# Optimization experiments

Hardware: AMD Instinct MI355X
Metric: run time of the kernel (lower is better)

## Reference

```python
import jax, jax.numpy as jnp
import numpy as np

N_HEADS = 32
D_IN = 128 + 256 + 1024  # 1408
D_HID = 256
D_OUT = 3


def setup_inputs() -> dict:
    key = jax.random.key(0)
    k1, k2, k3, k4, k5 = jax.random.split(key, 5)
    B = 16384
    total_feat = jax.random.normal(k1, (B, D_IN), dtype=jnp.float32)
    # Stacked per-head parameters. Original zero-inits the second Linear;
    # we use small random values so the baseline exercises non-trivial math.
    s1 = 1.0 / np.sqrt(D_IN)
    s2 = 1.0 / np.sqrt(D_HID)
    W1 = jax.random.uniform(k2, (N_HEADS, D_IN, D_HID), jnp.float32, -s1, s1)
    b1 = jax.random.uniform(k3, (N_HEADS, D_HID), jnp.float32, -s1, s1)
    W2 = jax.random.uniform(k4, (N_HEADS, D_HID, D_OUT), jnp.float32, -s2, s2)
    b2 = jax.random.uniform(k5, (N_HEADS, D_OUT), jnp.float32, -s2, s2)
    return {"total_feat": total_feat, "W1": W1, "b1": b1, "W2": W2, "b2": b2}


def reference(total_feat, W1, b1, W2, b2):
    # 32 heads of Linear(1408->256) -> ReLU -> Linear(256->3), batched.
    h = jax.nn.relu(jnp.einsum('bf,hfo->bho', total_feat, W1) + b1)  # [B,32,256]
    out = jnp.einsum('bho,hop->bhp', h, W2) + b2                     # [B,32,3]
    B = total_feat.shape[0]
    # concat(dim=-1) over heads == reshape since each head emits 3 contiguous values
    return out.reshape(B, N_HEADS * D_OUT)                           # [B,96]
```

## Files before the change

### kernel.cpp

```cpp
#include <hip/hip_runtime.h>
#include <hip/hip_bf16.h>
#include <stdint.h>

#define D_IN    1408
#define D_HID   256
#define N_HEADS 32
#define BATCH   16384

#define BM 64
#define BN 256
#define BK 64
#define KTILES (D_IN / BK)

typedef unsigned short u16;
typedef short short8 __attribute__((ext_vector_type(8)));
typedef float f32x4 __attribute__((ext_vector_type(4)));

__device__ __forceinline__ u16 f2b(float f) {
  __hip_bfloat16 h = __float2bfloat16(f);
  return *(u16*)&h;
}

__device__ __forceinline__ void gload_lds16(const void* g, void* l) {
  __builtin_amdgcn_global_load_lds(
      (const __attribute__((address_space(1))) uint32_t*)((const uint32_t*)g),
      (__attribute__((address_space(3))) uint32_t*)((uint32_t*)l),
      16, 0, 0);
}

__global__ void convert_x(const float4* __restrict__ X, ushort4* __restrict__ Xb) {
  int i = blockIdx.x * blockDim.x + threadIdx.x;
  float4 v = X[i];
  ushort4 o;
  o.x = f2b(v.x); o.y = f2b(v.y); o.z = f2b(v.z); o.w = f2b(v.w);
  Xb[i] = o;
}

__global__ void transpose_w1(const float* __restrict__ W1, u16* __restrict__ W1T) {
  __shared__ u16 tile[64][65];
  const int h = blockIdx.z;
  const int f0 = blockIdx.x * 64;
  const int o0 = blockIdx.y * 64;
  const int tx = threadIdx.x;
  const int ty = threadIdx.y;
  const size_t ib = (size_t)h * D_IN * D_HID;
  #pragma unroll
  for (int i = ty; i < 64; i += 4)
    tile[i][tx] = f2b(W1[ib + (size_t)(f0 + i) * D_HID + o0 + tx]);
  __syncthreads();
  const size_t ob = (size_t)h * D_HID * D_IN;
  #pragma unroll
  for (int i = ty; i < 64; i += 4)
    W1T[ob + (size_t)(o0 + i) * D_IN + f0 + tx] = tile[tx][i];
}

__global__ __launch_bounds__(256, 4) void mano_gemm(
    const u16* __restrict__ X,
    const u16* __restrict__ W1T,
    const float* __restrict__ b1,
    const float* __restrict__ W2,
    const float* __restrict__ b2,
    float* __restrict__ out)
{
  __shared__ __align__(16) u16 As[BM * BK];
  __shared__ __align__(16) u16 Bs[BN * BK];

  const int tid  = threadIdx.x;
  const int lane = tid & 63;
  const int wid  = tid >> 6;
  const int quad = lane >> 4;
  const int l15  = lane & 15;

  const int id    = blockIdx.x;
  const int xcd   = id & 7;
  const int s     = id >> 3;
  const int head  = xcd * 4 + (s & 3);
  const int mtile = s >> 2;
  const int m0    = mtile * BM;

  const u16* Au = X + (size_t)m0 * D_IN;
  const u16* Bu = W1T + (size_t)head * D_HID * D_IN;

  int aoff[2];
  #pragma unroll
  for (int c = 0; c < 2; ++c) {
    int ci  = c * 256 + wid * 64 + lane;
    int row = ci >> 3;
    int k8  = (ci & 7) ^ (row & 7);
    aoff[c] = row * D_IN + k8 * 8;
  }
  int boff[8];
  #pragma unroll
  for (int c = 0; c < 8; ++c) {
    int ci  = c * 256 + wid * 64 + lane;
    int row = ci >> 3;
    int k8  = (ci & 7) ^ (row & 7);
    boff[c] = row * D_IN + k8 * 8;
  }

  f32x4 acc[4][4];
  #pragma unroll
  for (int i = 0; i < 4; ++i)
    #pragma unroll
    for (int j = 0; j < 4; ++j)
      acc[i][j] = f32x4{0.f, 0.f, 0.f, 0.f};

  int arow[4], brow[4];
  #pragma unroll
  for (int i = 0; i < 4; ++i) {
    arow[i] = i * 16 + l15;
    brow[i] = wid * 64 + i * 16 + l15;
  }

  for (int kt = 0; kt < KTILES; ++kt) {
    const int kb = kt * BK;
    __syncthreads();
    #pragma unroll
    for (int c = 0; c < 2; ++c)
      gload_lds16(Au + aoff[c] + kb, As + (c * 256 + wid * 64) * 8);
    #pragma unroll
    for (int c = 0; c < 8; ++c)
      gload_lds16(Bu + boff[c] + kb, Bs + (c * 256 + wid * 64) * 8);
    __builtin_amdgcn_s_waitcnt(0x0F70);
    __syncthreads();

    #pragma unroll
    for (int ks = 0; ks < 2; ++ks) {
      short8 af[4], bfr[4];
      #pragma unroll
      for (int i = 0; i < 4; ++i) {
        int k8a = (ks * 4 + quad) ^ (arow[i] & 7);
        af[i]  = *(const short8*)((const char*)As + arow[i] * 128 + k8a * 16);
        int k8b = (ks * 4 + quad) ^ (brow[i] & 7);
        bfr[i] = *(const short8*)((const char*)Bs + brow[i] * 128 + k8b * 16);
      }
      #pragma unroll
      for (int i = 0; i < 4; ++i)
        #pragma unroll
        for (int j = 0; j < 4; ++j)
          acc[i][j] = __builtin_amdgcn_mfma_f32_16x16x32_bf16(af[i], bfr[j], acc[i][j], 0, 0, 0);
    }
  }

  const float* b1h = b1 + head * D_HID;
  const float* W2h = W2 + (size_t)head * D_HID * 3;

  float b1v[4], w2v[4][3];
  #pragma unroll
  for (int j = 0; j < 4; ++j) {
    int n = brow[j];
    b1v[j] = b1h[n];
    #pragma unroll
    for (int p = 0; p < 3; ++p)
      w2v[j][p] = W2h[n * 3 + p];
  }

  __syncthreads();
  float* scr = (float*)As;

  #pragma unroll
  for (int i = 0; i < 4; ++i) {
    float ps[4][3];
    #pragma unroll
    for (int r = 0; r < 4; ++r)
      #pragma unroll
      for (int p = 0; p < 3; ++p) ps[r][p] = 0.f;

    #pragma unroll
    for (int j = 0; j < 4; ++j)
      #pragma unroll
      for (int r = 0; r < 4; ++r) {
        float h = acc[i][j][r] + b1v[j];
        h = h > 0.f ? h : 0.f;
        #pragma unroll
        for (int p = 0; p < 3; ++p)
          ps[r][p] = fmaf(h, w2v[j][p], ps[r][p]);
      }

    #pragma unroll
    for (int mask = 1; mask < 16; mask <<= 1)
      #pragma unroll
      for (int r = 0; r < 4; ++r)
        #pragma unroll
        for (int p = 0; p < 3; ++p)
          ps[r][p] += __shfl_xor(ps[r][p], mask, 64);

    if (l15 == 0) {
      int row = i * 16 + quad * 4;
      #pragma unroll
      for (int r = 0; r < 4; ++r)
        #pragma unroll
        for (int p = 0; p < 3; ++p)
          scr[wid * 192 + (row + r) * 3 + p] = ps[r][p];
    }
  }
  __syncthreads();

  if (tid < 192) {
    int rl = tid / 3, p = tid - rl * 3;
    float v = scr[rl * 3 + p] + scr[192 + rl * 3 + p]
            + scr[384 + rl * 3 + p] + scr[576 + rl * 3 + p]
            + b2[head * 3 + p];
    out[(size_t)(m0 + rl) * (N_HEADS * 3) + head * 3 + p] = v;
  }
}

extern "C" void kernel_launch(void* const* d_in, const int* in_sizes, int n_in,
                              void* d_out, int out_size, void* d_ws, size_t ws_size,
                              hipStream_t stream) {
  const float* X  = (const float*)d_in[0];
  const float* W1 = (const float*)d_in[1];
  const float* b1 = (const float*)d_in[2];
  const float* W2 = (const float*)d_in[3];
  const float* b2 = (const float*)d_in[4];

  u16* Xb  = (u16*)d_ws;
  u16* W1T = (u16*)((char*)d_ws + (size_t)BATCH * D_IN * 2);

  convert_x<<<(BATCH * D_IN / 4) / 256, 256, 0, stream>>>(
      (const float4*)X, (ushort4*)Xb);

  transpose_w1<<<dim3(D_IN / 64, D_HID / 64, N_HEADS), dim3(64, 4), 0, stream>>>(W1, W1T);

  mano_gemm<<<dim3(BATCH / BM * N_HEADS), 256, 0, stream>>>(
      Xb, W1T, b1, W2, b2, (float*)d_out);
}
```

Measured before the change: 604.8 us.

## Enlarge GEMM tile to 256x256 with double-buffered LDS and interleaved MFMA phases

The tile grows from 64x256 to 256x256, the block from 256 to 512 threads (8 waves in a 2x4 grid), and LDS becomes double-buffered so global-to-LDS loads for the next K tiles overlap MFMA work. Each K iteration is split into four phases that alternate fragment loads, staged async copies, barriers and setprio around MFMA batches. The aim is more reuse of each loaded A and B element per MFMA and hidden global load latency. In exchange it uses more registers and LDS (128 KB), lowers occupancy, launches fewer blocks, and relies on fragile hand-counted vmcnt waits.

```diff
diff --git a/kernel.cpp b/kernel.cpp
--- a/kernel.cpp
+++ b/kernel.cpp
@@ -7,7 +7,7 @@
 #define N_HEADS 32
 #define BATCH   16384
 
-#define BM 64
+#define BM 256
 #define BN 256
 #define BK 64
 #define KTILES (D_IN / BK)
@@ -54,7 +54,7 @@
     W1T[ob + (size_t)(o0 + i) * D_IN + f0 + tx] = tile[tx][i];
 }
 
-__global__ __launch_bounds__(256, 4) void mano_gemm(
+__global__ __launch_bounds__(512, 2) void mano_gemm(
     const u16* __restrict__ X,
     const u16* __restrict__ W1T,
     const float* __restrict__ b1,
@@ -62,14 +62,16 @@
     const float* __restrict__ b2,
     float* __restrict__ out)
 {
-  __shared__ __align__(16) u16 As[BM * BK];
-  __shared__ __align__(16) u16 Bs[BN * BK];
+  __shared__ __align__(16) u16 As[2][BM * BK];
+  __shared__ __align__(16) u16 Bs[2][BN * BK];
 
   const int tid  = threadIdx.x;
   const int lane = tid & 63;
   const int wid  = tid >> 6;
   const int quad = lane >> 4;
   const int l15  = lane & 15;
+  const int wm   = wid >> 2;
+  const int wn   = wid & 3;
 
   const int id    = blockIdx.x;
   const int xcd   = id & 7;
@@ -81,85 +83,163 @@
   const u16* Au = X + (size_t)m0 * D_IN;
   const u16* Bu = W1T + (size_t)head * D_HID * D_IN;
 
-  int aoff[2];
+  int off[2][2];
   #pragma unroll
   for (int c = 0; c < 2; ++c) {
-    int ci  = c * 256 + wid * 64 + lane;
-    int row = ci >> 3;
-    int k8  = (ci & 7) ^ (row & 7);
-    aoff[c] = row * D_IN + k8 * 8;
-  }
-  int boff[8];
-  #pragma unroll
-  for (int c = 0; c < 8; ++c) {
-    int ci  = c * 256 + wid * 64 + lane;
-    int row = ci >> 3;
-    int k8  = (ci & 7) ^ (row & 7);
-    boff[c] = row * D_IN + k8 * 8;
-  }
-
-  f32x4 acc[4][4];
-  #pragma unroll
-  for (int i = 0; i < 4; ++i)
+    int ci = c * 512 + tid;
+    int rl = ci >> 3;
+    int k8 = (ci & 7) ^ (rl & 7);
+    #pragma unroll
+    for (int h = 0; h < 2; ++h)
+      off[h][c] = (h * 128 + rl) * D_IN + k8 * 8;
+  }
+
+#define STAGE_A(bufi, h, kt) do {                                          \
+    _Pragma("unroll")                                                      \
+    for (int c = 0; c < 2; ++c)                                            \
+      gload_lds16(Au + off[h][c] + (kt) * BK,                              \
+                  &As[bufi][((h) * 1024 + c * 512 + wid * 64) * 8]);       \
+  } while (0)
+#define STAGE_B(bufi, h, kt) do {                                          \
+    _Pragma("unroll")                                                      \
+    for (int c = 0; c < 2; ++c)                                            \
+      gload_lds16(Bu + off[h][c] + (kt) * BK,                              \
+                  &Bs[bufi][((h) * 1024 + c * 512 + wid * 64) * 8]);       \
+  } while (0)
+
+  const int wm16l = wm * 16 + l15;
+  const int wn16l = wn * 16 + l15;
+  const int rx  = l15 & 7;
+  const int co0 = (quad ^ rx) * 16;
+  const int co1 = ((4 + quad) ^ rx) * 16;
+
+#define LDA_FRAG(mf, ks) \
+  (*(const short8*)(Ab + ((mf) * 32 + wm16l) * 128 + ((ks) ? co1 : co0)))
+#define LDB_FRAG(nf, ks) \
+  (*(const short8*)(Bb + (nf) * 8192 + wn16l * 128 + ((ks) ? co1 : co0)))
+
+  f32x4 acc[8][4];
+  #pragma unroll
+  for (int i = 0; i < 8; ++i)
     #pragma unroll
     for (int j = 0; j < 4; ++j)
       acc[i][j] = f32x4{0.f, 0.f, 0.f, 0.f};
 
-  int arow[4], brow[4];
-  #pragma unroll
-  for (int i = 0; i < 4; ++i) {
-    arow[i] = i * 16 + l15;
-    brow[i] = wid * 64 + i * 16 + l15;
-  }
-
-  for (int kt = 0; kt < KTILES; ++kt) {
-    const int kb = kt * BK;
-    __syncthreads();
-    #pragma unroll
-    for (int c = 0; c < 2; ++c)
-      gload_lds16(Au + aoff[c] + kb, As + (c * 256 + wid * 64) * 8);
-    #pragma unroll
-    for (int c = 0; c < 8; ++c)
-      gload_lds16(Bu + boff[c] + kb, Bs + (c * 256 + wid * 64) * 8);
-    __builtin_amdgcn_s_waitcnt(0x0F70);
-    __syncthreads();
-
-    #pragma unroll
-    for (int ks = 0; ks < 2; ++ks) {
-      short8 af[4], bfr[4];
-      #pragma unroll
-      for (int i = 0; i < 4; ++i) {
-        int k8a = (ks * 4 + quad) ^ (arow[i] & 7);
-        af[i]  = *(const short8*)((const char*)As + arow[i] * 128 + k8a * 16);
-        int k8b = (ks * 4 + quad) ^ (brow[i] & 7);
-        bfr[i] = *(const short8*)((const char*)Bs + brow[i] * 128 + k8b * 16);
-      }
-      #pragma unroll
-      for (int i = 0; i < 4; ++i)
-        #pragma unroll
-        for (int j = 0; j < 4; ++j)
-          acc[i][j] = __builtin_amdgcn_mfma_f32_16x16x32_bf16(af[i], bfr[j], acc[i][j], 0, 0, 0);
-    }
-  }
+  STAGE_A(0, 0, 0);
+  STAGE_B(0, 1, 0);
+  STAGE_A(0, 1, 0);
+  STAGE_B(0, 0, 0);
+  STAGE_A(1, 0, 1);
+  STAGE_B(1, 1, 1);
+  asm volatile("s_waitcnt vmcnt(4)" ::: "memory");
+  __builtin_amdgcn_s_barrier();
+
+  short8 a[4][2], b[4][2];
+
+  for (int t = 0; t < KTILES; ++t) {
+    const int buf = t & 1;
+    const char* Ab = (const char*)&As[buf][0];
+    const char* Bb = (const char*)&Bs[buf][0];
+
+    #pragma unroll
+    for (int mf = 0; mf < 4; ++mf) {
+      a[mf][0] = LDA_FRAG(mf, 0);
+      a[mf][1] = LDA_FRAG(mf, 1);
+    }
+    #pragma unroll
+    for (int nf = 0; nf < 2; ++nf) {
+      b[nf][0] = LDB_FRAG(nf, 0);
+      b[nf][1] = LDB_FRAG(nf, 1);
+    }
+    if (t + 1 < KTILES) STAGE_A(buf ^ 1, 1, t + 1);
+    __builtin_amdgcn_s_barrier();
+    __builtin_amdgcn_s_setprio(1);
+    #pragma unroll
+    for (int mf = 0; mf < 4; ++mf)
+      #pragma unroll
+      for (int nf = 0; nf < 2; ++nf) {
+        acc[mf][nf] = __builtin_amdgcn_mfma_f32_16x16x32_bf16(a[mf][0], b[nf][0], acc[mf][nf], 0, 0, 0);
+        acc[mf][nf] = __builtin_amdgcn_mfma_f32_16x16x32_bf16(a[mf][1], b[nf][1], acc[mf][nf], 0, 0, 0);
+      }
+    __builtin_amdgcn_s_setprio(0);
+    __builtin_amdgcn_s_barrier();
+
+    #pragma unroll
+    for (int nf = 2; nf < 4; ++nf) {
+      b[nf][0] = LDB_FRAG(nf, 0);
+      b[nf][1] = LDB_FRAG(nf, 1);
+    }
+    if (t + 1 < KTILES) STAGE_B(buf ^ 1, 0, t + 1);
+    __builtin_amdgcn_s_barrier();
+    __builtin_amdgcn_s_setprio(1);
+    #pragma unroll
+    for (int mf = 0; mf < 4; ++mf)
+      #pragma unroll
+      for (int nf = 2; nf < 4; ++nf) {
+        acc[mf][nf] = __builtin_amdgcn_mfma_f32_16x16x32_bf16(a[mf][0], b[nf][0], acc[mf][nf], 0, 0, 0);
+        acc[mf][nf] = __builtin_amdgcn_mfma_f32_16x16x32_bf16(a[mf][1], b[nf][1], acc[mf][nf], 0, 0, 0);
+      }
+    __builtin_amdgcn_s_setprio(0);
+    __builtin_amdgcn_s_barrier();
+
+    #pragma unroll
+    for (int i = 0; i < 4; ++i) {
+      a[i][0] = LDA_FRAG(4 + i, 0);
+      a[i][1] = LDA_FRAG(4 + i, 1);
+    }
+    if (t + 2 < KTILES) STAGE_A(buf, 0, t + 2);
+    __builtin_amdgcn_s_barrier();
+    __builtin_amdgcn_s_setprio(1);
+    #pragma unroll
+    for (int i = 0; i < 4; ++i)
+      #pragma unroll
+      for (int nf = 2; nf < 4; ++nf) {
+        acc[4 + i][nf] = __builtin_amdgcn_mfma_f32_16x16x32_bf16(a[i][0], b[nf][0], acc[4 + i][nf], 0, 0, 0);
+        acc[4 + i][nf] = __builtin_amdgcn_mfma_f32_16x16x32_bf16(a[i][1], b[nf][1], acc[4 + i][nf], 0, 0, 0);
+      }
+    __builtin_amdgcn_s_setprio(0);
+    __builtin_amdgcn_s_barrier();
+
+    if (t + 2 < KTILES) STAGE_B(buf, 1, t + 2);
+    __builtin_amdgcn_s_barrier();
+    __builtin_amdgcn_s_setprio(1);
+    #pragma unroll
+    for (int i = 0; i < 4; ++i)
+      #pragma unroll
+      for (int nf = 0; nf < 2; ++nf) {
+        acc[4 + i][nf] = __builtin_amdgcn_mfma_f32_16x16x32_bf16(a[i][0], b[nf][0], acc[4 + i][nf], 0, 0, 0);
+        acc[4 + i][nf] = __builtin_amdgcn_mfma_f32_16x16x32_bf16(a[i][1], b[nf][1], acc[4 + i][nf], 0, 0, 0);
+      }
+    __builtin_amdgcn_s_setprio(0);
+    if (t < KTILES - 2) {
+      asm volatile("s_waitcnt vmcnt(4)" ::: "memory");
+    } else {
+      asm volatile("s_waitcnt vmcnt(0)" ::: "memory");
+    }
+    __builtin_amdgcn_s_barrier();
+  }
+
+#undef STAGE_A
+#undef STAGE_B
+#undef LDA_FRAG
+#undef LDB_FRAG
 
   const float* b1h = b1 + head * D_HID;
   const float* W2h = W2 + (size_t)head * D_HID * 3;
 
   float b1v[4], w2v[4][3];
   #pragma unroll
-  for (int j = 0; j < 4; ++j) {
-    int n = brow[j];
-    b1v[j] = b1h[n];
-    #pragma unroll
-    for (int p = 0; p < 3; ++p)
-      w2v[j][p] = W2h[n * 3 + p];
-  }
-
-  __syncthreads();
-  float* scr = (float*)As;
-
-  #pragma unroll
-  for (int i = 0; i < 4; ++i) {
+  for (int nf = 0; nf < 4; ++nf) {
+    int col = nf * 64 + wn16l;
+    b1v[nf] = b1h[col];
+    #pragma unroll
+    for (int p = 0; p < 3; ++p) w2v[nf][p] = W2h[col * 3 + p];
+  }
+
+  float* scr = (float*)&As[0][0];
+
+  #pragma unroll
+  for (int mf = 0; mf < 8; ++mf) {
     float ps[4][3];
     #pragma unroll
     for (int r = 0; r < 4; ++r)
@@ -167,14 +247,14 @@
       for (int p = 0; p < 3; ++p) ps[r][p] = 0.f;
 
     #pragma unroll
-    for (int j = 0; j < 4; ++j)
+    for (int nf = 0; nf < 4; ++nf)
       #pragma unroll
       for (int r = 0; r < 4; ++r) {
-        float h = acc[i][j][r] + b1v[j];
+        float h = acc[mf][nf][r] + b1v[nf];
         h = h > 0.f ? h : 0.f;
         #pragma unroll
         for (int p = 0; p < 3; ++p)
-          ps[r][p] = fmaf(h, w2v[j][p], ps[r][p]);
+          ps[r][p] = fmaf(h, w2v[nf][p], ps[r][p]);
       }
 
     #pragma unroll
@@ -186,22 +266,21 @@
           ps[r][p] += __shfl_xor(ps[r][p], mask, 64);
 
     if (l15 == 0) {
-      int row = i * 16 + quad * 4;
+      int row = mf * 32 + wm * 16 + quad * 4;
       #pragma unroll
       for (int r = 0; r < 4; ++r)
         #pragma unroll
         for (int p = 0; p < 3; ++p)
-          scr[wid * 192 + (row + r) * 3 + p] = ps[r][p];
+          scr[((row + r) * 3 + p) * 4 + wn] = ps[r][p];
     }
   }
   __syncthreads();
 
-  if (tid < 192) {
-    int rl = tid / 3, p = tid - rl * 3;
-    float v = scr[rl * 3 + p] + scr[192 + rl * 3 + p]
-            + scr[384 + rl * 3 + p] + scr[576 + rl * 3 + p]
+  for (int i = tid; i < BM * 3; i += 512) {
+    int row = i / 3, p = i - row * 3;
+    float v = scr[i * 4 + 0] + scr[i * 4 + 1] + scr[i * 4 + 2] + scr[i * 4 + 3]
             + b2[head * 3 + p];
-    out[(size_t)(m0 + rl) * (N_HEADS * 3) + head * 3 + p] = v;
+    out[(size_t)(m0 + row) * (N_HEADS * 3) + head * 3 + p] = v;
   }
 }
 
@@ -222,6 +301,6 @@
 
   transpose_w1<<<dim3(D_IN / 64, D_HID / 64, N_HEADS), dim3(64, 4), 0, stream>>>(W1, W1T);
 
-  mano_gemm<<<dim3(BATCH / BM * N_HEADS), 256, 0, stream>>>(
+  mano_gemm<<<dim3(BATCH / BM * N_HEADS), 512, 0, stream>>>(
       Xb, W1T, b1, W2, b2, (float*)d_out);
 }
```

Result: faster. 553.0 us (-8.6%).

## Persistent 256x256 double-buffered GEMM with interleaved loads and MFMA phases

Applied to the files above, without the earlier changes.

Replaces the 64x256 single-buffered tile kernel with a persistent 512-thread kernel that computes 256x256 tiles. Each block loops over 8 M-segments for a fixed head. LDS is double-buffered, and global-to-LDS loads for the next k-tile, including the next segment's first tiles, are interleaved with MFMA phases using barriers and setprio. Bias and W2 are staged in LDS, and the W1 transpose now writes vectorized ushort4. The aim is to remove per-tile load stalls and raise arithmetic intensity, at the cost of heavy register pressure from 32 accumulators and complex wait-count logic.

```diff
diff --git a/kernel.cpp b/kernel.cpp
--- a/kernel.cpp
+++ b/kernel.cpp
@@ -7,10 +7,11 @@
 #define N_HEADS 32
 #define BATCH   16384
 
-#define BM 64
+#define BM 256
 #define BN 256
 #define BK 64
 #define KTILES (D_IN / BK)
+#define NSEG 8
 
 typedef unsigned short u16;
 typedef short short8 __attribute__((ext_vector_type(8)));
@@ -37,7 +38,7 @@
 }
 
 __global__ void transpose_w1(const float* __restrict__ W1, u16* __restrict__ W1T) {
-  __shared__ u16 tile[64][65];
+  __shared__ u16 tile[64][68];
   const int h = blockIdx.z;
   const int f0 = blockIdx.x * 64;
   const int o0 = blockIdx.y * 64;
@@ -50,11 +51,17 @@
   __syncthreads();
   const size_t ob = (size_t)h * D_HID * D_IN;
   #pragma unroll
-  for (int i = ty; i < 64; i += 4)
-    W1T[ob + (size_t)(o0 + i) * D_IN + f0 + tx] = tile[tx][i];
-}
-
-__global__ __launch_bounds__(256, 4) void mano_gemm(
+  for (int pass = 0; pass < 4; ++pass) {
+    int r = pass * 16 + ty * 4 + (tx >> 4);
+    int c = (tx & 15) * 4;
+    ushort4 v;
+    v.x = tile[c + 0][r]; v.y = tile[c + 1][r];
+    v.z = tile[c + 2][r]; v.w = tile[c + 3][r];
+    *(ushort4*)&W1T[ob + (size_t)(o0 + r) * D_IN + f0 + c] = v;
+  }
+}
+
+__global__ __launch_bounds__(512, 2) void mano_gemm(
     const u16* __restrict__ X,
     const u16* __restrict__ W1T,
     const float* __restrict__ b1,
@@ -62,147 +69,235 @@
     const float* __restrict__ b2,
     float* __restrict__ out)
 {
-  __shared__ __align__(16) u16 As[BM * BK];
-  __shared__ __align__(16) u16 Bs[BN * BK];
+  __shared__ __align__(16) u16 As[2][BM * BK];
+  __shared__ __align__(16) u16 Bs[2][BN * BK];
+  __shared__ __align__(16) float scr[3072];
+  __shared__ float b1L[256];
+  __shared__ float w2L[768];
+  __shared__ float b2L[3];
 
   const int tid  = threadIdx.x;
   const int lane = tid & 63;
   const int wid  = tid >> 6;
   const int quad = lane >> 4;
   const int l15  = lane & 15;
-
-  const int id    = blockIdx.x;
-  const int xcd   = id & 7;
-  const int s     = id >> 3;
-  const int head  = xcd * 4 + (s & 3);
-  const int mtile = s >> 2;
-  const int m0    = mtile * BM;
-
-  const u16* Au = X + (size_t)m0 * D_IN;
+  const int wm   = wid >> 2;
+  const int wn   = wid & 3;
+
+  const int bid  = blockIdx.x;
+  const int head = (bid & 7) * 4 + ((bid >> 3) & 3);
+  const int u2   = bid >> 5;
+
   const u16* Bu = W1T + (size_t)head * D_HID * D_IN;
 
-  int aoff[2];
+  if (tid < 256) b1L[tid] = b1[head * D_HID + tid];
+  for (int i = tid; i < 768; i += 512) w2L[i] = W2[(size_t)head * D_HID * 3 + i];
+  if (tid < 3)  b2L[tid] = b2[head * 3 + tid];
+
+  int off[2][2];
   #pragma unroll
   for (int c = 0; c < 2; ++c) {
-    int ci  = c * 256 + wid * 64 + lane;
-    int row = ci >> 3;
-    int k8  = (ci & 7) ^ (row & 7);
-    aoff[c] = row * D_IN + k8 * 8;
+    int ci = c * 512 + tid;
+    int rl = ci >> 3;
+    int k8 = (ci & 7) ^ (rl & 7);
+    #pragma unroll
+    for (int h = 0; h < 2; ++h)
+      off[h][c] = (h * 128 + rl) * D_IN + k8 * 8;
   }
-  int boff[8];
+
+#define STG_A(BI, H, P) do { _Pragma("unroll")                                 \
+    for (int c = 0; c < 2; ++c)                                                \
+      gload_lds16((P) + off[H][c],                                             \
+                  &As[BI][((H) * 1024 + c * 512 + wid * 64) * 8]); } while (0)
+#define STG_B(BI, H, P) do { _Pragma("unroll")                                 \
+    for (int c = 0; c < 2; ++c)                                                \
+      gload_lds16((P) + off[H][c],                                             \
+                  &Bs[BI][((H) * 1024 + c * 512 + wid * 64) * 8]); } while (0)
+
+  const int wm16l = wm * 16 + l15;
+  const int wn16l = wn * 16 + l15;
+  const int rx  = l15 & 7;
+  const int co0 = (quad ^ rx) * 16;
+  const int co1 = ((4 + quad) ^ rx) * 16;
+
+#define LDAF(BI, mf, ks)                                                       \
+  (*(const short8*)((const char*)&As[BI][0] +                                  \
+                    ((mf) * 32 + wm16l) * 128 + ((ks) ? co1 : co0)))
+#define LDBF(BI, nf, ks)                                                       \
+  (*(const short8*)((const char*)&Bs[BI][0] +                                  \
+                    (nf) * 8192 + wn16l * 128 + ((ks) ? co1 : co0)))
+#define MM(mi, nj, ks)                                                         \
+  acc[mi][nj] = __builtin_amdgcn_mfma_f32_16x16x32_bf16(                       \
+      a[(mi) & 3][ks], b[nj][ks], acc[mi][nj], 0, 0, 0)
+
+  f32x4 acc[8][4];
   #pragma unroll
-  for (int c = 0; c < 8; ++c) {
-    int ci  = c * 256 + wid * 64 + lane;
-    int row = ci >> 3;
-    int k8  = (ci & 7) ^ (row & 7);
-    boff[c] = row * D_IN + k8 * 8;
-  }
-
-  f32x4 acc[4][4];
-  #pragma unroll
-  for (int i = 0; i < 4; ++i)
+  for (int i = 0; i < 8; ++i)
     #pragma unroll
     for (int j = 0; j < 4; ++j)
       acc[i][j] = f32x4{0.f, 0.f, 0.f, 0.f};
 
-  int arow[4], brow[4];
-  #pragma unroll
-  for (int i = 0; i < 4; ++i) {
-    arow[i] = i * 16 + l15;
-    brow[i] = wid * 64 + i * 16 + l15;
+  short8 a[4][2], b[4][2];
+
+#define DO_TILE(BI, B0P, B0SK, A0P, A0SK, B1P, B1SK, A1P, A1SK, DRAIN)         \
+  do {                                                                         \
+              \
+    _Pragma("unroll") for (int mf = 0; mf < 4; ++mf) {                         \
+      a[mf][0] = LDAF(BI, mf, 0); a[mf][1] = LDAF(BI, mf, 1); }                \
+    _Pragma("unroll") for (int nf = 0; nf < 2; ++nf) {                         \
+      b[nf][0] = LDBF(BI, nf, 0); b[nf][1] = LDBF(BI, nf, 1); }                \
+    if (!(B0SK)) STG_B((BI) ^ 1, 0, B0P);                                      \
+    __builtin_amdgcn_s_barrier();                                              \
+    __builtin_amdgcn_s_setprio(1);                                             \
+    _Pragma("unroll") for (int mf = 0; mf < 4; ++mf) {                         \
+      MM(mf, 0, 0); MM(mf, 0, 1); MM(mf, 1, 0); MM(mf, 1, 1); }                \
+    __builtin_amdgcn_s_setprio(0);                                             \
+    __builtin_amdgcn_s_barrier();                                              \
+         \
+    _Pragma("unroll") for (int nf = 2; nf < 4; ++nf) {                         \
+      b[nf][0] = LDBF(BI, nf, 0); b[nf][1] = LDBF(BI, nf, 1); }                \
+    if (!(A0SK)) STG_A(BI, 0, A0P);                                            \
+    __builtin_amdgcn_s_barrier();                                              \
+    __builtin_amdgcn_s_setprio(1);                                             \
+    _Pragma("unroll") for (int mf = 0; mf < 4; ++mf) {                         \
+      MM(mf, 2, 0); MM(mf, 2, 1); MM(mf, 3, 0); MM(mf, 3, 1); }                \
+    __builtin_amdgcn_s_setprio(0);                                             \
+    __builtin_amdgcn_s_barrier();                                              \
+         \
+    _Pragma("unroll") for (int i = 0; i < 4; ++i) {                            \
+      a[i][0] = LDAF(BI, 4 + i, 0); a[i][1] = LDAF(BI, 4 + i, 1); }            \
+    if (!(B1SK)) STG_B(BI, 1, B1P);                                            \
+    __builtin_amdgcn_s_barrier();                                              \
+    __builtin_amdgcn_s_setprio(1);                                             \
+    _Pragma("unroll") for (int i = 0; i < 4; ++i) {                            \
+      MM(4 + i, 2, 0); MM(4 + i, 2, 1); MM(4 + i, 3, 0); MM(4 + i, 3, 1); }    \
+    __builtin_amdgcn_s_setprio(0);                                             \
+    __builtin_amdgcn_s_barrier();                                              \
+                     \
+    if (!(A1SK)) STG_A(BI, 1, A1P);                                            \
+    __builtin_amdgcn_s_barrier();                                              \
+    __builtin_amdgcn_s_setprio(1);                                             \
+    _Pragma("unroll") for (int i = 0; i < 4; ++i) {                            \
+      MM(4 + i, 0, 0); MM(4 + i, 0, 1); MM(4 + i, 1, 0); MM(4 + i, 1, 1); }    \
+    __builtin_amdgcn_s_setprio(0);                                             \
+    if (DRAIN) { asm volatile("s_waitcnt vmcnt(0)" ::: "memory"); }            \
+    else       { asm volatile("s_waitcnt vmcnt(6)" ::: "memory"); }            \
+    __builtin_amdgcn_s_barrier();                                              \
+  } while (0)
+
+  {
+    const u16* Au0 = X + (size_t)(u2 * 256) * D_IN;
+    STG_A(0, 0, Au0);
+    STG_B(0, 1, Bu);
+    STG_A(0, 1, Au0);
+    STG_B(0, 0, Bu);
+    STG_A(1, 0, Au0 + BK);
+    STG_B(1, 1, Bu + BK);
+    STG_A(1, 1, Au0 + BK);
+    asm volatile("s_waitcnt lgkmcnt(0)" ::: "memory");
+    asm volatile("s_waitcnt vmcnt(6)" ::: "memory");
+    __builtin_amdgcn_s_barrier();
   }
 
-  for (int kt = 0; kt < KTILES; ++kt) {
-    const int kb = kt * BK;
-    __syncthreads();
-    #pragma unroll
-    for (int c = 0; c < 2; ++c)
-      gload_lds16(Au + aoff[c] + kb, As + (c * 256 + wid * 64) * 8);
-    #pragma unroll
-    for (int c = 0; c < 8; ++c)
-      gload_lds16(Bu + boff[c] + kb, Bs + (c * 256 + wid * 64) * 8);
-    __builtin_amdgcn_s_waitcnt(0x0F70);
-    __syncthreads();
-
-    #pragma unroll
-    for (int ks = 0; ks < 2; ++ks) {
-      short8 af[4], bfr[4];
+  #pragma unroll 1
+  for (int g = 0; g < NSEG; ++g) {
+    const u16* AuC = X + (size_t)((g * 8 + u2) * 256) * D_IN;
+    const u16* AuN = AuC + (size_t)(8 * 256) * D_IN;
+    const bool lastseg = (g == NSEG - 1);
+
+    #pragma unroll 1
+    for (int j = 0; j < KTILES / 2; ++j) {
+      const int kt0 = 2 * j;
+      const int kp1 = kt0 + 1;
+      const int kp2 = kt0 + 2;
+      const int kp3 = kt0 + 3;
+      const bool w2f = (kp2 >= KTILES), w3f = (kp3 >= KTILES);
+      const int k2m = w2f ? kp2 - KTILES : kp2;
+      const int k3m = w3f ? kp3 - KTILES : kp3;
+      const u16* Bp1 = Bu + kp1 * BK;
+      const u16* Bp2 = Bu + k2m * BK;
+      const u16* Bp3 = Bu + k3m * BK;
+      const u16* Ap2 = (w2f ? AuN : AuC) + k2m * BK;
+      const u16* Ap3 = (w3f ? AuN : AuC) + k3m * BK;
+      const bool sk2 = lastseg && w2f;
+      const bool sk3 = lastseg && w3f;
+      const bool drain = lastseg && (j == KTILES / 2 - 1);
+
+      DO_TILE(0, Bp1, false, Ap2, sk2, Bp2, sk2, Ap2, sk2, drain);
+      DO_TILE(1, Bp2, sk2,   Ap3, sk3, Bp3, sk3, Ap3, sk3, drain);
+    }
+
+    {
+      float b1v[4], w2v[4][3];
       #pragma unroll
-      for (int i = 0; i < 4; ++i) {
-        int k8a = (ks * 4 + quad) ^ (arow[i] & 7);
-        af[i]  = *(const short8*)((const char*)As + arow[i] * 128 + k8a * 16);
-        int k8b = (ks * 4 + quad) ^ (brow[i] & 7);
-        bfr[i] = *(const short8*)((const char*)Bs + brow[i] * 128 + k8b * 16);
+      for (int nf = 0; nf < 4; ++nf) {
+        int col = nf * 64 + wn16l;
+        b1v[nf] = b1L[col];
+        #pragma unroll
+        for (int p = 0; p < 3; ++p) w2v[nf][p] = w2L[col * 3 + p];
       }
+      const int m0 = (g * 8 + u2) * 256;
+
       #pragma unroll
-      for (int i = 0; i < 4; ++i)
-        #pragma unroll
-        for (int j = 0; j < 4; ++j)
-          acc[i][j] = __builtin_amdgcn_mfma_f32_16x16x32_bf16(af[i], bfr[j], acc[i][j], 0, 0, 0);
+      for (int mf = 0; mf < 8; ++mf) {
+        float ps[4][3];
+        #pragma unroll
+        for (int r = 0; r < 4; ++r)
+          #pragma unroll
+          for (int p = 0; p < 3; ++p) ps[r][p] = 0.f;
+
+        #pragma unroll
+        for (int nf = 0; nf < 4; ++nf)
+          #pragma unroll
+          for (int r = 0; r < 4; ++r) {
+            float h = acc[mf][nf][r] + b1v[nf];
+            h = h > 0.f ? h : 0.f;
+            #pragma unroll
+            for (int p = 0; p < 3; ++p)
+              ps[r][p] = fmaf(h, w2v[nf][p], ps[r][p]);
+          }
+
+        #pragma unroll
+        for (int mask = 1; mask < 16; mask <<= 1)
+          #pragma unroll
+          for (int r = 0; r < 4; ++r)
+            #pragma unroll
+            for (int p = 0; p < 3; ++p)
+              ps[r][p] += __shfl_xor(ps[r][p], mask, 64);
+
+        if (l15 == 0) {
+          int row = mf * 32 + wm * 16 + quad * 4;
+          #pragma unroll
+          for (int r = 0; r < 4; ++r)
+            #pragma unroll
+            for (int p = 0; p < 3; ++p)
+              scr[((row + r) * 3 + p) * 4 + wn] = ps[r][p];
+        }
+      }
+      asm volatile("s_waitcnt lgkmcnt(0)" ::: "memory");
+      __builtin_amdgcn_s_barrier();
+
+      for (int i = tid; i < BM * 3; i += 512) {
+        int row = i / 3, p = i - row * 3;
+        float v = scr[i * 4 + 0] + scr[i * 4 + 1] + scr[i * 4 + 2]
+                + scr[i * 4 + 3] + b2L[p];
+        out[(size_t)(m0 + row) * (N_HEADS * 3) + head * 3 + p] = v;
+      }
+
+      #pragma unroll
+      for (int i = 0; i < 8; ++i)
+        #pragma unroll
+        for (int jj = 0; jj < 4; ++jj)
+          acc[i][jj] = f32x4{0.f, 0.f, 0.f, 0.f};
     }
   }
 
-  const float* b1h = b1 + head * D_HID;
-  const float* W2h = W2 + (size_t)head * D_HID * 3;
-
-  float b1v[4], w2v[4][3];
-  #pragma unroll
-  for (int j = 0; j < 4; ++j) {
-    int n = brow[j];
-    b1v[j] = b1h[n];
-    #pragma unroll
-    for (int p = 0; p < 3; ++p)
-      w2v[j][p] = W2h[n * 3 + p];
-  }
-
-  __syncthreads();
-  float* scr = (float*)As;
-
-  #pragma unroll
-  for (int i = 0; i < 4; ++i) {
-    float ps[4][3];
-    #pragma unroll
-    for (int r = 0; r < 4; ++r)
-      #pragma unroll
-      for (int p = 0; p < 3; ++p) ps[r][p] = 0.f;
-
-    #pragma unroll
-    for (int j = 0; j < 4; ++j)
-      #pragma unroll
-      for (int r = 0; r < 4; ++r) {
-        float h = acc[i][j][r] + b1v[j];
-        h = h > 0.f ? h : 0.f;
-        #pragma unroll
-        for (int p = 0; p < 3; ++p)
-          ps[r][p] = fmaf(h, w2v[j][p], ps[r][p]);
-      }
-
-    #pragma unroll
-    for (int mask = 1; mask < 16; mask <<= 1)
-      #pragma unroll
-      for (int r = 0; r < 4; ++r)
-        #pragma unroll
-        for (int p = 0; p < 3; ++p)
-          ps[r][p] += __shfl_xor(ps[r][p], mask, 64);
-
-    if (l15 == 0) {
-      int row = i * 16 + quad * 4;
-      #pragma unroll
-      for (int r = 0; r < 4; ++r)
-        #pragma unroll
-        for (int p = 0; p < 3; ++p)
-          scr[wid * 192 + (row + r) * 3 + p] = ps[r][p];
-    }
-  }
-  __syncthreads();
-
-  if (tid < 192) {
-    int rl = tid / 3, p = tid - rl * 3;
-    float v = scr[rl * 3 + p] + scr[192 + rl * 3 + p]
-            + scr[384 + rl * 3 + p] + scr[576 + rl * 3 + p]
-            + b2[head * 3 + p];
-    out[(size_t)(m0 + rl) * (N_HEADS * 3) + head * 3 + p] = v;
-  }
+#undef STG_A
+#undef STG_B
+#undef LDAF
+#undef LDBF
+#undef MM
+#undef DO_TILE
 }
 
 extern "C" void kernel_launch(void* const* d_in, const int* in_sizes, int n_in,
@@ -222,6 +317,6 @@
 
   transpose_w1<<<dim3(D_IN / 64, D_HID / 64, N_HEADS), dim3(64, 4), 0, stream>>>(W1, W1T);
 
-  mano_gemm<<<dim3(BATCH / BM * N_HEADS), 256, 0, stream>>>(
+  mano_gemm<<<dim3(256), 512, 0, stream>>>(
       Xb, W1T, b1, W2, b2, (float*)d_out);
 }
```

Result: faster. 552.7 us (-8.6%).
